# Performance work log

Hardware: AMD Instinct MI355X
Metric: run time of the kernel (lower is better)

## Reference

```python
import jax, jax.numpy as jnp
import numpy as np

SIZE = 48          # sinkhorn_canvas_size
EPS = 0.01         # entropy regularization
ITERS = 5          # sinkhorn iterations
CHANNEL = 0        # fixed channel (original picks a random one of 3)


def _build_cost_matrix(size):
    y, x = jnp.meshgrid(jnp.arange(size), jnp.arange(size), indexing='ij')
    pixels = jnp.stack((y.flatten(), x.flatten()), axis=1).astype(jnp.float32) / size  # [N,2]
    diff = pixels[:, None, :] - pixels[None, :, :]  # [N,N,2]
    return jnp.sum(diff * diff, axis=-1)            # [N,N]


def setup_inputs() -> dict:
    key = jax.random.key(0)
    k1, k2 = jax.random.split(key)
    B = 32
    img_pred = jax.random.uniform(k1, (B, 3, SIZE, SIZE), dtype=jnp.float32)
    img_target = jax.random.uniform(k2, (B, 3, SIZE, SIZE), dtype=jnp.float32)
    cost_matrix = _build_cost_matrix(SIZE)
    return {"img_pred": img_pred, "img_target": img_target, "cost_matrix": cost_matrix}


def reference(img_pred, img_target, cost_matrix):
    B = img_pred.shape[0]
    # fixed channel, flatten spatial dims -> [B, N]
    p = img_pred[:, CHANNEL].reshape(B, -1) + 1e-9
    t = img_target[:, CHANNEL].reshape(B, -1) + 1e-9
    mass_source = p / jnp.sum(p, axis=-1, keepdims=True)
    mass_target = t / jnp.sum(t, axis=-1, keepdims=True)
    log_u = jnp.log(mass_source)
    log_v = jnp.log(mass_target)
    u = jnp.zeros_like(mass_source)
    v = jnp.zeros_like(mass_target)

    def M(u, v):
        # modified cost for log-domain updates: [B, N, N]
        return (-cost_matrix[None, :, :] + u[:, :, None] + v[:, None, :]) / EPS

    def lse(A):
        # matches torch: log(sum(exp(A), axis=2) + 1e-6)
        return jnp.log(jnp.sum(jnp.exp(A), axis=2) + 1e-6)

    for _ in range(ITERS):
        u = EPS * (log_u - lse(M(u, v))) + u
        v = EPS * (log_v - lse(jnp.swapaxes(M(u, v), 1, 2))) + v

    P = jnp.exp(M(u, v))                               # [B, N, N]
    cost = jnp.sum(P * cost_matrix[None, :, :], axis=(1, 2))  # [B]
    return cost
```

## Files before the change

kernel.cpp:

```cpp
#include <hip/hip_runtime.h>


#define SZ 48
#define SN 2304
#define LD 49
#define NBAT 32
#define NTHR 384
#define YB 8

__global__ __launch_bounds__(256) void k_pre(const float* __restrict__ C,
                                             float* __restrict__ G,
                                             float* __restrict__ H) {
    for (int idx = threadIdx.x; idx < SN; idx += 256) {
        const int a = idx / SZ;
        const int c = idx - a * SZ;
        const float cv = C[(size_t)a * SZ * SN + (size_t)c * SZ];
        const float g = expf(-100.f * cv);
        G[idx] = g;
        H[idx] = g * cv;
    }
}

__global__ __launch_bounds__(NTHR) void k_sink(const float* __restrict__ pred,
                                               const float* __restrict__ tgt,
                                               const float* __restrict__ Gm,
                                               const float* __restrict__ Hm,
                                               float* __restrict__ out) {
    __shared__ float Fa[SZ * LD];
    __shared__ float Fb[SZ * LD];
    __shared__ float Fms[SZ * LD];
    __shared__ float Fmt[SZ * LD];
    __shared__ float T[SZ * LD];
    __shared__ float red[16];

    const int t = threadIdx.x;
    const int b = blockIdx.x;
    const int l = t & 63;
    const int w = __builtin_amdgcn_readfirstlane(t >> 6);
    const int r0 = w * YB;

    const float* __restrict__ pg = pred + (size_t)b * 3 * SN;
    const float* __restrict__ tg = tgt + (size_t)b * 3 * SN;
    float sp = 0.f, st = 0.f;
    for (int i = t; i < SN; i += NTHR) {
        const float vp = pg[i] + 1e-9f;
        const float vt = tg[i] + 1e-9f;
        const int y = i / SZ, x = i - y * SZ;
        Fms[y * LD + x] = vp;
        Fmt[y * LD + x] = vt;
        sp += vp; st += vt;
    }
    #pragma unroll
    for (int off = 32; off; off >>= 1) {
        sp += __shfl_down(sp, off);
        st += __shfl_down(st, off);
    }
    if (l == 0) { red[w] = sp; red[8 + w] = st; }
    __syncthreads();
    float ps = 0.f, ts = 0.f;
    #pragma unroll
    for (int k = 0; k < 6; ++k) { ps += red[k]; ts += red[8 + k]; }
    for (int i = t; i < SN; i += NTHR) {
        const int y = i / SZ, x = i - y * SZ;
        Fms[y * LD + x] /= ps;
        Fmt[y * LD + x] /= ts;
        Fa[y * LD + x] = 1.f;
        Fb[y * LD + x] = 1.f;
    }
    __syncthreads();

    for (int p = 0; p < 10; ++p) {
        float* __restrict__ src = (p & 1) ? Fa : Fb;
        float* __restrict__ dst = (p & 1) ? Fb : Fa;
        const float* __restrict__ mv = (p & 1) ? Fmt : Fms;

        if (l < SZ) {
            float acc[YB];
            #pragma unroll
            for (int k = 0; k < YB; ++k) acc[k] = 0.f;
            #pragma unroll 4
            for (int j = 0; j < SZ; ++j) {
                const float v = src[l * LD + j];
                #pragma unroll
                for (int k = 0; k < YB; ++k)
                    acc[k] = fmaf(Gm[j * SZ + r0 + k], v, acc[k]);
            }
            #pragma unroll
            for (int k = 0; k < YB; ++k) T[l * LD + r0 + k] = acc[k];
        }
        __syncthreads();

        if (l < SZ) {
            float acc[YB];
            #pragma unroll
            for (int k = 0; k < YB; ++k) acc[k] = 0.f;
            #pragma unroll 4
            for (int j = 0; j < SZ; ++j) {
                const float v = T[j * LD + l];
                #pragma unroll
                for (int k = 0; k < YB; ++k)
                    acc[k] = fmaf(Gm[j * SZ + r0 + k], v, acc[k]);
            }
            #pragma unroll
            for (int k = 0; k < YB; ++k) {
                const int idx = (r0 + k) * LD + l;
                const float yo = dst[idx];
                dst[idx] = mv[idx] * yo / (yo * acc[k] + 1e-6f);
            }
        }
        __syncthreads();
    }

    if (l < SZ) {
        float t1[YB], t2[YB];
        #pragma unroll
        for (int k = 0; k < YB; ++k) { t1[k] = 0.f; t2[k] = 0.f; }
        #pragma unroll 2
        for (int j = 0; j < SZ; ++j) {
            const float v = Fb[l * LD + j];
            #pragma unroll
            for (int k = 0; k < YB; ++k) {
                t1[k] = fmaf(Gm[j * SZ + r0 + k], v, t1[k]);
                t2[k] = fmaf(Hm[j * SZ + r0 + k], v, t2[k]);
            }
        }
        #pragma unroll
        for (int k = 0; k < YB; ++k) {
            T[l * LD + r0 + k]   = t1[k];
            Fms[l * LD + r0 + k] = t2[k];
        }
    }
    __syncthreads();

    float part = 0.f;
    if (l < SZ) {
        float u[YB];
        #pragma unroll
        for (int k = 0; k < YB; ++k) u[k] = 0.f;
        #pragma unroll 2
        for (int j = 0; j < SZ; ++j) {
            const float v1 = T[j * LD + l];
            const float v2 = Fms[j * LD + l];
            #pragma unroll
            for (int k = 0; k < YB; ++k) {
                u[k] = fmaf(Hm[j * SZ + r0 + k], v1, u[k]);
                u[k] = fmaf(Gm[j * SZ + r0 + k], v2, u[k]);
            }
        }
        #pragma unroll
        for (int k = 0; k < YB; ++k)
            part = fmaf(Fa[(r0 + k) * LD + l], u[k], part);
    }
    #pragma unroll
    for (int off = 32; off; off >>= 1) part += __shfl_down(part, off);
    if (l == 0) red[w] = part;
    __syncthreads();
    if (t == 0) {
        float c = 0.f;
        #pragma unroll
        for (int k = 0; k < 6; ++k) c += red[k];
        out[b] = c;
    }
}

extern "C" void kernel_launch(void* const* d_in, const int* in_sizes, int n_in,
                              void* d_out, int out_size, void* d_ws, size_t ws_size,
                              hipStream_t stream) {
    const float* pred = (const float*)d_in[0];
    const float* tgt  = (const float*)d_in[1];
    const float* C    = (const float*)d_in[2];
    float* G = (float*)d_ws;
    float* H = G + SN;

    k_pre<<<1, 256, 0, stream>>>(C, G, H);
    k_sink<<<NBAT, NTHR, 0, stream>>>(pred, tgt, G, H, (float*)d_out);
}
```

Measured before the change: 120.2 us.

## Fuse precompute into single kernel and keep Sinkhorn scalings in registers with readlane broadcasts

Merges the separate cost-factor precompute kernel into the main Sinkhorn kernel, so each block builds the 1D Gaussian factor from the cost matrix in shared memory. The scaling vectors now live in registers, six rows per wave across eight waves, and are broadcast with readlane instead of being read from shared memory. The first half-iteration is computed in closed form from the all-ones start, which saves one separable pass. The aim is to remove a kernel launch, shared-memory traffic and barriers, at the cost of heavy register use (48-element Gc plus float4 arrays) and redundant precompute in every block.

```diff
diff --git a/kernel.cpp b/kernel.cpp
--- a/kernel.cpp
+++ b/kernel.cpp
@@ -3,52 +3,112 @@
 
 #define SZ 48
 #define SN 2304
-#define LD 49
+#define LDT 52
 #define NBAT 32
-#define NTHR 384
-#define YB 8
-
-__global__ __launch_bounds__(256) void k_pre(const float* __restrict__ C,
-                                             float* __restrict__ G,
-                                             float* __restrict__ H) {
-    for (int idx = threadIdx.x; idx < SN; idx += 256) {
-        const int a = idx / SZ;
-        const int c = idx - a * SZ;
-        const float cv = C[(size_t)a * SZ * SN + (size_t)c * SZ];
-        const float g = expf(-100.f * cv);
-        G[idx] = g;
-        H[idx] = g * cv;
-    }
-}
-
-__global__ __launch_bounds__(NTHR) void k_sink(const float* __restrict__ pred,
-                                               const float* __restrict__ tgt,
-                                               const float* __restrict__ Gm,
-                                               const float* __restrict__ Hm,
-                                               float* __restrict__ out) {
-    __shared__ float Fa[SZ * LD];
-    __shared__ float Fb[SZ * LD];
-    __shared__ float Fms[SZ * LD];
-    __shared__ float Fmt[SZ * LD];
-    __shared__ float T[SZ * LD];
+#define NTHR 512
+#define NW 8
+#define QB 6
+
+__device__ __forceinline__ float rl(float v, int j) {
+    return __int_as_float(__builtin_amdgcn_readlane(__float_as_int(v), j));
+}
+
+__device__ __forceinline__ float getc(const float4 v, int i) {
+    return i == 0 ? v.x : i == 1 ? v.y : i == 2 ? v.z : v.w;
+}
+
+__device__ __forceinline__ void half_iter(const float* __restrict__ Gc,
+                                          const float* __restrict__ Grow,
+                                          const float* __restrict__ src,
+                                          float* __restrict__ dst,
+                                          const float* __restrict__ mv,
+                                          float* __restrict__ TT,
+                                          int l, int lc, int r0) {
+    float ac[QB];
+    #pragma unroll
+    for (int q = 0; q < QB; ++q) ac[q] = 0.f;
+    #pragma unroll
+    for (int j = 0; j < SZ; ++j) {
+        #pragma unroll
+        for (int q = 0; q < QB; ++q)
+            ac[q] = fmaf(Gc[j], rl(src[q], j), ac[q]);
+    }
+    if (l < SZ) {
+        *(float2*)&TT[lc * LDT + r0    ] = make_float2(ac[0], ac[1]);
+        *(float2*)&TT[lc * LDT + r0 + 2] = make_float2(ac[2], ac[3]);
+        *(float2*)&TT[lc * LDT + r0 + 4] = make_float2(ac[4], ac[5]);
+    }
+    __syncthreads();
+    float4 qv[12];
+    #pragma unroll
+    for (int jc = 0; jc < 12; ++jc)
+        qv[jc] = *(const float4*)&TT[lc * LDT + jc * 4];
+    float s2[QB];
+    #pragma unroll
+    for (int q = 0; q < QB; ++q) s2[q] = 0.f;
+    #pragma unroll
+    for (int j = 0; j < SZ; ++j) {
+        const float tj = getc(qv[j >> 2], j & 3);
+        #pragma unroll
+        for (int q = 0; q < QB; ++q)
+            s2[q] = fmaf(rl(Grow[q], j), tj, s2[q]);
+    }
+    #pragma unroll
+    for (int q = 0; q < QB; ++q) {
+        const float yo = dst[q];
+        dst[q] = mv[q] * yo / (yo * s2[q] + 1e-6f);
+    }
+}
+
+__global__ __launch_bounds__(NTHR, 1) void k_all(const float* __restrict__ pred,
+                                                 const float* __restrict__ tgt,
+                                                 const float* __restrict__ C,
+                                                 float* __restrict__ out) {
+    __shared__ float LC[SZ * LDT];
+    __shared__ float TA[SZ * LDT];
+    __shared__ float TB[SZ * LDT];
     __shared__ float red[16];
 
     const int t = threadIdx.x;
     const int b = blockIdx.x;
     const int l = t & 63;
-    const int w = __builtin_amdgcn_readfirstlane(t >> 6);
-    const int r0 = w * YB;
+    const int w = t >> 6;
+    const int r0 = w * QB;
+    const int lc = (l < SZ) ? l : 0;
+
+    for (int i = t; i < SN; i += NTHR) {
+        const int a = i / SZ, c = i - a * SZ;
+        const float cv = C[(size_t)a * SZ * SN + (size_t)c * SZ];
+        LC[a * LDT + c] = cv;
+        TA[a * LDT + c] = expf(-100.f * cv);
+    }
+    __syncthreads();
+
+    float Gc[SZ];
+    #pragma unroll
+    for (int j = 0; j < SZ; ++j) Gc[j] = TA[j * LDT + lc];
+    float Grow[QB], Crow[QB];
+    #pragma unroll
+    for (int q = 0; q < QB; ++q) {
+        Grow[q] = TA[(r0 + q) * LDT + lc];
+        Crow[q] = LC[(r0 + q) * LDT + lc];
+    }
+    float gs = 0.f;
+    #pragma unroll
+    for (int j = 0; j < SZ; ++j) gs += Gc[j];
 
     const float* __restrict__ pg = pred + (size_t)b * 3 * SN;
     const float* __restrict__ tg = tgt + (size_t)b * 3 * SN;
+    float ms[QB], mt[QB];
+    #pragma unroll
+    for (int q = 0; q < QB; ++q) {
+        ms[q] = pg[(r0 + q) * SZ + lc] + 1e-9f;
+        mt[q] = tg[(r0 + q) * SZ + lc] + 1e-9f;
+    }
     float sp = 0.f, st = 0.f;
-    for (int i = t; i < SN; i += NTHR) {
-        const float vp = pg[i] + 1e-9f;
-        const float vt = tg[i] + 1e-9f;
-        const int y = i / SZ, x = i - y * SZ;
-        Fms[y * LD + x] = vp;
-        Fmt[y * LD + x] = vt;
-        sp += vp; st += vt;
+    if (l < SZ) {
+        #pragma unroll
+        for (int q = 0; q < QB; ++q) { sp += ms[q]; st += mt[q]; }
     }
     #pragma unroll
     for (int off = 32; off; off >>= 1) {
@@ -59,97 +119,84 @@
     __syncthreads();
     float ps = 0.f, ts = 0.f;
     #pragma unroll
-    for (int k = 0; k < 6; ++k) { ps += red[k]; ts += red[8 + k]; }
-    for (int i = t; i < SN; i += NTHR) {
-        const int y = i / SZ, x = i - y * SZ;
-        Fms[y * LD + x] /= ps;
-        Fmt[y * LD + x] /= ts;
-        Fa[y * LD + x] = 1.f;
-        Fb[y * LD + x] = 1.f;
-    }
-    __syncthreads();
-
-    for (int p = 0; p < 10; ++p) {
-        float* __restrict__ src = (p & 1) ? Fa : Fb;
-        float* __restrict__ dst = (p & 1) ? Fb : Fa;
-        const float* __restrict__ mv = (p & 1) ? Fmt : Fms;
-
+    for (int k = 0; k < NW; ++k) { ps += red[k]; ts += red[8 + k]; }
+
+    float Fa[QB], Fb[QB];
+    #pragma unroll
+    for (int q = 0; q < QB; ++q) {
+        ms[q] /= ps;
+        mt[q] /= ts;
+        const float gr = rl(gs, r0 + q);
+        Fa[q] = ms[q] / (gr * gs + 1e-6f);
+        Fb[q] = 1.f;
+    }
+
+    #pragma unroll 1
+    for (int it = 0; it < 4; ++it) {
+        half_iter(Gc, Grow, Fa, Fb, mt, TA, l, lc, r0);
+        half_iter(Gc, Grow, Fb, Fa, ms, TB, l, lc, r0);
+    }
+    half_iter(Gc, Grow, Fa, Fb, mt, TA, l, lc, r0);
+    __syncthreads();
+
+    {
+        float4 cq[12];
+        #pragma unroll
+        for (int jc = 0; jc < 12; ++jc)
+            cq[jc] = *(const float4*)&LC[lc * LDT + jc * 4];
+        float t1[QB], t2[QB];
+        #pragma unroll
+        for (int q = 0; q < QB; ++q) { t1[q] = 0.f; t2[q] = 0.f; }
+        #pragma unroll
+        for (int j = 0; j < SZ; ++j) {
+            const float cc = getc(cq[j >> 2], j & 3);
+            const float hc = Gc[j] * cc;
+            #pragma unroll
+            for (int q = 0; q < QB; ++q) {
+                const float s = rl(Fb[q], j);
+                t1[q] = fmaf(Gc[j], s, t1[q]);
+                t2[q] = fmaf(hc,    s, t2[q]);
+            }
+        }
         if (l < SZ) {
-            float acc[YB];
+            *(float2*)&TA[lc * LDT + r0    ] = make_float2(t1[0], t1[1]);
+            *(float2*)&TA[lc * LDT + r0 + 2] = make_float2(t1[2], t1[3]);
+            *(float2*)&TA[lc * LDT + r0 + 4] = make_float2(t1[4], t1[5]);
+            *(float2*)&TB[lc * LDT + r0    ] = make_float2(t2[0], t2[1]);
+            *(float2*)&TB[lc * LDT + r0 + 2] = make_float2(t2[2], t2[3]);
+            *(float2*)&TB[lc * LDT + r0 + 4] = make_float2(t2[4], t2[5]);
+        }
+    }
+    __syncthreads();
+
+    float part = 0.f;
+    {
+        float4 q1[12], q2[12];
+        #pragma unroll
+        for (int jc = 0; jc < 12; ++jc) {
+            q1[jc] = *(const float4*)&TA[lc * LDT + jc * 4];
+            q2[jc] = *(const float4*)&TB[lc * LDT + jc * 4];
+        }
+        float Hrow[QB];
+        #pragma unroll
+        for (int q = 0; q < QB; ++q) Hrow[q] = Grow[q] * Crow[q];
+        float u[QB];
+        #pragma unroll
+        for (int q = 0; q < QB; ++q) u[q] = 0.f;
+        #pragma unroll
+        for (int j = 0; j < SZ; ++j) {
+            const float a1 = getc(q1[j >> 2], j & 3);
+            const float a2 = getc(q2[j >> 2], j & 3);
             #pragma unroll
-            for (int k = 0; k < YB; ++k) acc[k] = 0.f;
-            #pragma unroll 4
-            for (int j = 0; j < SZ; ++j) {
-                const float v = src[l * LD + j];
-                #pragma unroll
-                for (int k = 0; k < YB; ++k)
-                    acc[k] = fmaf(Gm[j * SZ + r0 + k], v, acc[k]);
+            for (int q = 0; q < QB; ++q) {
+                u[q] = fmaf(rl(Hrow[q], j), a1, u[q]);
+                u[q] = fmaf(rl(Grow[q], j), a2, u[q]);
             }
+        }
+        if (l < SZ) {
             #pragma unroll
-            for (int k = 0; k < YB; ++k) T[l * LD + r0 + k] = acc[k];
-        }
-        __syncthreads();
-
-        if (l < SZ) {
-            float acc[YB];
-            #pragma unroll
-            for (int k = 0; k < YB; ++k) acc[k] = 0.f;
-            #pragma unroll 4
-            for (int j = 0; j < SZ; ++j) {
-                const float v = T[j * LD + l];
-                #pragma unroll
-                for (int k = 0; k < YB; ++k)
-                    acc[k] = fmaf(Gm[j * SZ + r0 + k], v, acc[k]);
-            }
-            #pragma unroll
-            for (int k = 0; k < YB; ++k) {
-                const int idx = (r0 + k) * LD + l;
-                const float yo = dst[idx];
-                dst[idx] = mv[idx] * yo / (yo * acc[k] + 1e-6f);
-            }
-        }
-        __syncthreads();
-    }
-
-    if (l < SZ) {
-        float t1[YB], t2[YB];
-        #pragma unroll
-        for (int k = 0; k < YB; ++k) { t1[k] = 0.f; t2[k] = 0.f; }
-        #pragma unroll 2
-        for (int j = 0; j < SZ; ++j) {
-            const float v = Fb[l * LD + j];
-            #pragma unroll
-            for (int k = 0; k < YB; ++k) {
-                t1[k] = fmaf(Gm[j * SZ + r0 + k], v, t1[k]);
-                t2[k] = fmaf(Hm[j * SZ + r0 + k], v, t2[k]);
-            }
-        }
-        #pragma unroll
-        for (int k = 0; k < YB; ++k) {
-            T[l * LD + r0 + k]   = t1[k];
-            Fms[l * LD + r0 + k] = t2[k];
-        }
-    }
-    __syncthreads();
-
-    float part = 0.f;
-    if (l < SZ) {
-        float u[YB];
-        #pragma unroll
-        for (int k = 0; k < YB; ++k) u[k] = 0.f;
-        #pragma unroll 2
-        for (int j = 0; j < SZ; ++j) {
-            const float v1 = T[j * LD + l];
-            const float v2 = Fms[j * LD + l];
-            #pragma unroll
-            for (int k = 0; k < YB; ++k) {
-                u[k] = fmaf(Hm[j * SZ + r0 + k], v1, u[k]);
-                u[k] = fmaf(Gm[j * SZ + r0 + k], v2, u[k]);
-            }
-        }
-        #pragma unroll
-        for (int k = 0; k < YB; ++k)
-            part = fmaf(Fa[(r0 + k) * LD + l], u[k], part);
+            for (int q = 0; q < QB; ++q) part = fmaf(Fa[q], u[q], part);
+        }
     }
     #pragma unroll
     for (int off = 32; off; off >>= 1) part += __shfl_down(part, off);
@@ -158,7 +205,7 @@
     if (t == 0) {
         float c = 0.f;
         #pragma unroll
-        for (int k = 0; k < 6; ++k) c += red[k];
+        for (int k = 0; k < NW; ++k) c += red[k];
         out[b] = c;
     }
 }
@@ -169,9 +216,5 @@
     const float* pred = (const float*)d_in[0];
     const float* tgt  = (const float*)d_in[1];
     const float* C    = (const float*)d_in[2];
-    float* G = (float*)d_ws;
-    float* H = G + SN;
-
-    k_pre<<<1, 256, 0, stream>>>(C, G, H);
-    k_sink<<<NBAT, NTHR, 0, stream>>>(pred, tgt, G, H, (float*)d_out);
-}
+    k_all<<<NBAT, NTHR, 0, stream>>>(pred, tgt, C, (float*)d_out);
+}
```

New measurement: 134.6 us. 12.0% more time.
